# Kernel optimization log

Measured on AMD Instinct MI355X. Metric: run time of the kernel, lower is better.

## Reference

```python
import jax, jax.numpy as jnp
import numpy as np

N, B, E = 2048, 2, 1024      # seq_len, batch, embedding_dims
H = 1024                      # hidden_dims
NH, D = 16, 64                # num_heads, head_dim (NH*D == H)
SCALE = 1.0 / float(np.sqrt(H))  # NOTE: module divides by sqrt(hidden_dims), not sqrt(head_dim)


def setup_inputs() -> dict:
    key = jax.random.key(0)
    k0, k1, k2 = jax.random.split(key, 3)
    x = jax.random.normal(k0, (N, B, E), dtype=jnp.float32)
    W_proj = jax.random.normal(k1, (E, 3 * H), dtype=jnp.float32) * 0.02
    b_proj = jnp.zeros((3 * H,), dtype=jnp.float32)
    W_out = jax.random.normal(k2, (H, E), dtype=jnp.float32) * 0.02
    b_out = jnp.zeros((E,), dtype=jnp.float32)
    return {"x": x, "W_proj": W_proj, "b_proj": b_proj, "W_out": W_out, "b_out": b_out}


def reference(x, W_proj, b_proj, W_out, b_out):
    n, b, _ = x.shape
    # QKV projection: [n, b, 3H] -> 'n b (k h d) -> k b h n d'
    proj = x @ W_proj + b_proj
    qkv = proj.reshape(n, b, 3, NH, D).transpose(2, 1, 3, 0, 4)  # [3, b, h, n, d]
    q, k, v = qkv[0], qkv[1], qkv[2]
    # scaled dot-product scores [b, h, n, n]
    scores = jnp.einsum('bhid,bhjd->bhij', q, k) * SCALE
    # causal mask: -inf above the diagonal (generate_square_subsequent_mask)
    i = jnp.arange(n)
    mask = jnp.where(i[None, :] > i[:, None], -jnp.inf, 0.0).astype(scores.dtype)
    att = jax.nn.softmax(scores + mask, axis=-1)  # dropout = identity (eval)
    out = jnp.einsum('bhij,bhjd->bhid', att, v)   # [b, h, n, d]
    out = out.transpose(2, 0, 1, 3).reshape(n, b, H)  # 'b h n d -> n b (h d)'
    return out @ W_out + b_out
```

## Files before the change

kernel.cpp:

```cpp
#include <hip/hip_runtime.h>
#include <cstdint>
#include <cstddef>

typedef __bf16 bf16_t;
typedef __bf16 bf16x8 __attribute__((ext_vector_type(8)));
typedef __bf16 bf16x4 __attribute__((ext_vector_type(4)));
typedef float f32x4 __attribute__((ext_vector_type(4)));

#define N_SEQ 2048
#define BATCH 2
#define EMB   1024
#define HID   1024
#define NHEAD 16
#define HDIM  64
#define NBROW (N_SEQ * BATCH)
#define ATT_SCALE2 (0.03125f * 1.44269504f)

#define EXP2F(x) __builtin_amdgcn_exp2f(x)

static __device__ __forceinline__ void async_copy16(const bf16_t* g, bf16_t* l) {
  __builtin_amdgcn_global_load_lds((const __attribute__((address_space(1))) void*)g,
                                   (__attribute__((address_space(3))) void*)l,
                                   16, 0, 0);
}

__global__ __launch_bounds__(256) void prep_kernel(
    const float* __restrict__ x, const float* __restrict__ Wp,
    const float* __restrict__ Wo, bf16_t* __restrict__ Xb,
    bf16_t* __restrict__ Wpt, bf16_t* __restrict__ Wot) {
  int bid = blockIdx.x;
  if (bid < 4096) {
    int i = (bid * 256 + threadIdx.x) * 4;
    float4 v = *(const float4*)(x + i);
    bf16x4 o;
    o[0] = (bf16_t)v.x; o[1] = (bf16_t)v.y; o[2] = (bf16_t)v.z; o[3] = (bf16_t)v.w;
    *(bf16x4*)(Xb + i) = o;
    return;
  }
  __shared__ float tile[32][33];
  const float* in; bf16_t* out; int R, C, bx;
  if (bid < 4096 + 3072) { bx = bid - 4096; in = Wp; out = Wpt; R = 1024; C = 3072; }
  else                   { bx = bid - 7168; in = Wo; out = Wot; R = 1024; C = 1024; }
  int gx = C / 32;
  int bc = (bx % gx) * 32, br = (bx / gx) * 32;
  int tx = threadIdx.x & 31, ty = threadIdx.x >> 5;
  #pragma unroll
  for (int i = 0; i < 32; i += 8)
    tile[ty + i][tx] = in[(size_t)(br + ty + i) * C + bc + tx];
  __syncthreads();
  #pragma unroll
  for (int i = 0; i < 32; i += 8)
    out[(size_t)(bc + ty + i) * R + br + tx] = (bf16_t)tile[tx][ty + i];
}

template <int BM, int BN, bool OUT_BF16, bool SCALEQ, bool WRITE_VT>
__global__ __launch_bounds__(256) void gemm_bt_kernel(
    const bf16_t* __restrict__ A, const bf16_t* __restrict__ Bt,
    const float* __restrict__ bias, void* __restrict__ Cout,
    bf16_t* __restrict__ Vt, int M, int Nn, int K) {
  constexpr int BK = 64;
  constexpr int MT = BM / 32;
  constexpr int NT = BN / 32;
  constexpr int CA = BM / 32;
  constexpr int CB = BN / 32;
  constexpr int ASZ = BM * BK;
  constexpr int BSZ = BN * BK;
  __shared__ __align__(16) bf16_t smem[2 * ASZ + 2 * BSZ];
  bf16_t* const Asb = smem;
  bf16_t* const Bsb = smem + 2 * ASZ;
  int tid = threadIdx.x;
  int wave = tid >> 6, lane = tid & 63;
  int c = lane & 15, quad = lane >> 4;
  int bm = blockIdx.x * BM;
  int bn = blockIdx.y * BN;
  int wm = (wave & 1) * (BM / 2), wn = (wave >> 1) * (BN / 2);
  f32x4 acc[MT][NT] = {};

  const bf16_t* agp[CA]; int alo[CA];
  const bf16_t* bgp[CB]; int blo[CB];
  #pragma unroll
  for (int i = 0; i < CA; ++i) {
    int p = i * 256 + tid;
    int row = p >> 3, ko = (p & 7) ^ (row & 7);
    agp[i] = A + (size_t)(bm + row) * K + ko * 8;
    alo[i] = (i * 256 + wave * 64) * 8;
  }
  #pragma unroll
  for (int i = 0; i < CB; ++i) {
    int p = i * 256 + tid;
    int row = p >> 3, ko = (p & 7) ^ (row & 7);
    bgp[i] = Bt + (size_t)(bn + row) * K + ko * 8;
    blo[i] = (i * 256 + wave * 64) * 8;
  }

  #pragma unroll
  for (int i = 0; i < CA; ++i) async_copy16(agp[i], Asb + alo[i]);
  #pragma unroll
  for (int i = 0; i < CB; ++i) async_copy16(bgp[i], Bsb + blo[i]);

  int nkb = K / BK;
  for (int ki = 0; ki < nkb; ++ki) {
    __syncthreads();
    if (ki + 1 < nkb) {
      int kb = (ki + 1) * BK;
      bf16_t* an = Asb + ((ki + 1) & 1) * ASZ;
      bf16_t* bnx = Bsb + ((ki + 1) & 1) * BSZ;
      #pragma unroll
      for (int i = 0; i < CA; ++i) async_copy16(agp[i] + kb, an + alo[i]);
      #pragma unroll
      for (int i = 0; i < CB; ++i) async_copy16(bgp[i] + kb, bnx + blo[i]);
    }
    const bf16_t* as = Asb + (ki & 1) * ASZ;
    const bf16_t* bs = Bsb + (ki & 1) * BSZ;
    #pragma unroll
    for (int kk = 0; kk < 2; ++kk) {
      bf16x8 af[MT], bf[NT];
      #pragma unroll
      for (int mt = 0; mt < MT; ++mt) {
        int row = wm + mt * 16 + c;
        int slot = (kk * 4 + quad) ^ (row & 7);
        af[mt] = *(const bf16x8*)(as + (size_t)(row * 8 + slot) * 8);
      }
      #pragma unroll
      for (int nt = 0; nt < NT; ++nt) {
        int row = wn + nt * 16 + c;
        int slot = (kk * 4 + quad) ^ (row & 7);
        bf[nt] = *(const bf16x8*)(bs + (size_t)(row * 8 + slot) * 8);
      }
      #pragma unroll
      for (int mt = 0; mt < MT; ++mt)
        #pragma unroll
        for (int nt = 0; nt < NT; ++nt)
          acc[mt][nt] = __builtin_amdgcn_mfma_f32_16x16x32_bf16(
              af[mt], bf[nt], acc[mt][nt], 0, 0, 0);
    }
  }

  bool do_vt = WRITE_VT && (bn >= 2 * HID);
  bf16_t* tb = smem;
  if (do_vt) __syncthreads();

  #pragma unroll
  for (int nt = 0; nt < NT; ++nt) {
    int col = bn + wn + nt * 16 + c;
    float bv = bias[col];
    float sc = (SCALEQ && col < HID) ? ATT_SCALE2 : 1.0f;
    #pragma unroll
    for (int mt = 0; mt < MT; ++mt) {
      #pragma unroll
      for (int r = 0; r < 4; ++r) {
        int loc = wm + mt * 16 + quad * 4 + r;
        int row = bm + loc;
        float v = (acc[mt][nt][r] + bv) * sc;
        if (OUT_BF16)
          ((bf16_t*)Cout)[(size_t)row * Nn + col] = (bf16_t)v;
        else
          ((float*)Cout)[(size_t)row * Nn + col] = v;
        if (do_vt) {
          int dg = wn + nt * 16 + c;
          int hh = dg >> 6, dl = dg & 63;
          tb[((loc & 1) * 2 + hh) * 4608 + dl * 72 + (loc >> 1)] = (bf16_t)v;
        }
      }
    }
  }

  if (do_vt) {
    __syncthreads();
    int h0 = (bn - 2 * HID) >> 6;
    int n2 = (tid & 7) * 8;
    #pragma unroll
    for (int i = 0; i < 2; ++i) {
      #pragma unroll
      for (int hh = 0; hh < 2; ++hh) {
        #pragma unroll
        for (int k = 0; k < 2; ++k) {
          int d = (tid >> 3) + k * 32;
          bf16x8 vv = *(const bf16x8*)(tb + ((i * 2 + hh) * 4608) + d * 72 + n2);
          *(bf16x8*)(Vt + (size_t)((i * 16 + h0 + hh) * HDIM + d) * N_SEQ + bm / 2 + n2) = vv;
        }
      }
    }
  }
}

__global__ __launch_bounds__(512, 4) void flash_attn_kernel(
    const bf16_t* __restrict__ Pj, const bf16_t* __restrict__ Vt,
    bf16_t* __restrict__ AO) {
  __shared__ __align__(16) bf16_t Ks[2][64 * 64];
  __shared__ __align__(16) bf16_t Vs[2][64 * 64];
  __shared__ __align__(16) bf16_t Ps[8][16 * 64];
  const int PJP = 3 * HID;
  int tid = threadIdx.x, wave = tid >> 6, lane = tid & 63;
  int c = lane & 15, quad = lane >> 4;
  int c7 = c & 7;
  int bid = blockIdx.x;
  int qb = (bid < 256) ? (15 - (bid >> 5)) : ((bid - 256) >> 5);
  int bh = bid & 31;
  int h = bh & 15, b = bh >> 4;
  int i0 = qb * 128;

  int i_row = i0 + wave * 16 + c;
  const bf16_t* qg = Pj + (size_t)(i_row * BATCH + b) * PJP + h * HDIM + quad * 8;
  bf16x8 qf0 = *(const bf16x8*)(qg);
  bf16x8 qf1 = *(const bf16x8*)(qg + 32);

  f32x4 o[4] = {};
  float lrow = 0.f;

  int jr = tid >> 3, oc = tid & 7;
  int lds_off = jr * 64 + (oc ^ (jr & 7)) * 8;
  const bf16_t* kg0 = Pj + (size_t)b * PJP + HID + h * HDIM + oc * 8;
  const bf16_t* vg0 = Vt + (size_t)(bh * HDIM + jr) * N_SEQ + oc * 8;

  int njt = 2 * qb + 2;
  bf16x8 kreg = *(const bf16x8*)(kg0 + (size_t)jr * BATCH * PJP);
  bf16x8 vreg = *(const bf16x8*)(vg0);

  for (int jt = 0; jt < njt; ++jt) {
    bf16_t* ks = Ks[jt & 1];
    bf16_t* vs = Vs[jt & 1];
    *(bf16x8*)(ks + lds_off) = kreg;
    *(bf16x8*)(vs + lds_off) = vreg;
    __syncthreads();
    if (jt + 1 < njt) {
      int j0n = (jt + 1) * 64;
      kreg = *(const bf16x8*)(kg0 + (size_t)(j0n + jr) * BATCH * PJP);
      vreg = *(const bf16x8*)(vg0 + j0n);
    }

    f32x4 st[4];
    #pragma unroll
    for (int mt = 0; mt < 4; ++mt) {
      const bf16_t* kr = ks + (mt * 16 + c) * 64;
      bf16x8 ka0 = *(const bf16x8*)(kr + ((quad) ^ c7) * 8);
      bf16x8 ka1 = *(const bf16x8*)(kr + ((quad + 4) ^ c7) * 8);
      f32x4 s = {};
      s = __builtin_amdgcn_mfma_f32_16x16x32_bf16(ka0, qf0, s, 0, 0, 0);
      st[mt] = __builtin_amdgcn_mfma_f32_16x16x32_bf16(ka1, qf1, s, 0, 0, 0);
    }
    if (jt >= 2 * qb) {
      int j0 = jt * 64;
      int ig = i0 + wave * 16 + c;
      #pragma unroll
      for (int mt = 0; mt < 4; ++mt)
        #pragma unroll
        for (int r = 0; r < 4; ++r)
          if (j0 + mt * 16 + quad * 4 + r > ig) st[mt][r] = -1e30f;
    }

    #pragma unroll
    for (int mt = 0; mt < 4; ++mt)
      #pragma unroll
      for (int r = 0; r < 4; ++r) {
        st[mt][r] = EXP2F(st[mt][r]);
        lrow += st[mt][r];
      }

    bf16_t* pw = Ps[wave];
    #pragma unroll
    for (int mt = 0; mt < 4; ++mt) {
      bf16x4 pv;
      #pragma unroll
      for (int r = 0; r < 4; ++r) pv[r] = (bf16_t)st[mt][r];
      int joct = mt * 2 + (quad >> 1);
      *(bf16x4*)(pw + c * 64 + (joct ^ c7) * 8 + (quad & 1) * 4) = pv;
    }
    const bf16_t* pr = pw + c * 64;
    bf16x8 pa0 = *(const bf16x8*)(pr + ((quad) ^ c7) * 8);
    bf16x8 pa1 = *(const bf16x8*)(pr + ((quad + 4) ^ c7) * 8);

    #pragma unroll
    for (int nt = 0; nt < 4; ++nt) {
      const bf16_t* vr = vs + (nt * 16 + c) * 64;
      bf16x8 vb0 = *(const bf16x8*)(vr + ((quad) ^ c7) * 8);
      bf16x8 vb1 = *(const bf16x8*)(vr + ((quad + 4) ^ c7) * 8);
      o[nt] = __builtin_amdgcn_mfma_f32_16x16x32_bf16(vb0, pa0, o[nt], 0, 0, 0);
      o[nt] = __builtin_amdgcn_mfma_f32_16x16x32_bf16(vb1, pa1, o[nt], 0, 0, 0);
    }
  }

  float lfull = lrow;
  lfull += __shfl_xor(lfull, 16);
  lfull += __shfl_xor(lfull, 32);
  float linv = 1.0f / lfull;
  int orow = (i0 + wave * 16 + c) * BATCH + b;
  #pragma unroll
  for (int nt = 0; nt < 4; ++nt) {
    bf16x4 pv;
    #pragma unroll
    for (int r = 0; r < 4; ++r) pv[r] = (bf16_t)(o[nt][r] * linv);
    *(bf16x4*)(AO + (size_t)orow * HID + h * HDIM + nt * 16 + quad * 4) = pv;
  }
}

extern "C" void kernel_launch(void* const* d_in, const int* in_sizes, int n_in,
                              void* d_out, int out_size, void* d_ws, size_t ws_size,
                              hipStream_t stream) {
  const float* x      = (const float*)d_in[0];
  const float* W_proj = (const float*)d_in[1];
  const float* b_proj = (const float*)d_in[2];
  const float* W_out  = (const float*)d_in[3];
  const float* b_out  = (const float*)d_in[4];

  bf16_t* Xb  = (bf16_t*)d_ws;
  bf16_t* Wpt = Xb  + (size_t)NBROW * EMB;
  bf16_t* Wot = Wpt + (size_t)3 * HID * EMB;
  bf16_t* Pj  = Wot + (size_t)HID * EMB;
  bf16_t* AO  = Pj  + (size_t)NBROW * 3 * HID;
  bf16_t* Vt  = AO  + (size_t)NBROW * HID;

  prep_kernel<<<8192, 256, 0, stream>>>(x, W_proj, W_out, Xb, Wpt, Wot);
  gemm_bt_kernel<128, 128, true, true, true>
      <<<dim3(NBROW / 128, 3 * HID / 128), 256, 0, stream>>>(
      Xb, Wpt, b_proj, (void*)Pj, Vt, NBROW, 3 * HID, EMB);
  flash_attn_kernel<<<512, 512, 0, stream>>>(Pj, Vt, AO);
  gemm_bt_kernel<128, 128, false, false, false>
      <<<dim3(NBROW / 128, EMB / 128), 256, 0, stream>>>(
      AO, Wot, b_out, d_out, nullptr, NBROW, EMB, HID);
}
```

Before: 160.8 us.

## Rewrite flash attention with 32x32 MFMA, register-resident P and causal tile skip

The attention kernel moves from 16x16x32 to 32x32x16 bf16 MFMA, with each of 4 waves owning 32 query rows instead of 8 waves with 16 rows each, so blocks use 256 threads. The probability tile is repacked into B-operand layout in registers with cross-half lane shuffles, which drops the per-wave LDS round trip for P. Waves skip key tiles that lie entirely above their causal diagonal, and s_setprio is raised around the MFMA bursts. The trade-off is more registers per wave and fewer waves per block, which may lower occupancy and latency hiding.

After: 171.5 us. 6.7% more time.

```diff
diff --git a/kernel.cpp b/kernel.cpp
--- a/kernel.cpp
+++ b/kernel.cpp
@@ -6,6 +6,8 @@
 typedef __bf16 bf16x8 __attribute__((ext_vector_type(8)));
 typedef __bf16 bf16x4 __attribute__((ext_vector_type(4)));
 typedef float f32x4 __attribute__((ext_vector_type(4)));
+typedef float f32x16 __attribute__((ext_vector_type(16)));
+typedef unsigned int u32x4 __attribute__((ext_vector_type(4)));
 
 #define N_SEQ 2048
 #define BATCH 2
@@ -184,113 +186,180 @@
   }
 }
 
-__global__ __launch_bounds__(512, 4) void flash_attn_kernel(
+__global__ __launch_bounds__(256, 3) void flash_attn_kernel(
     const bf16_t* __restrict__ Pj, const bf16_t* __restrict__ Vt,
     bf16_t* __restrict__ AO) {
   __shared__ __align__(16) bf16_t Ks[2][64 * 64];
   __shared__ __align__(16) bf16_t Vs[2][64 * 64];
-  __shared__ __align__(16) bf16_t Ps[8][16 * 64];
   const int PJP = 3 * HID;
   int tid = threadIdx.x, wave = tid >> 6, lane = tid & 63;
-  int c = lane & 15, quad = lane >> 4;
-  int c7 = c & 7;
+  int il = lane & 31, half = lane >> 5;
   int bid = blockIdx.x;
   int qb = (bid < 256) ? (15 - (bid >> 5)) : ((bid - 256) >> 5);
   int bh = bid & 31;
   int h = bh & 15, b = bh >> 4;
   int i0 = qb * 128;
-
-  int i_row = i0 + wave * 16 + c;
-  const bf16_t* qg = Pj + (size_t)(i_row * BATCH + b) * PJP + h * HDIM + quad * 8;
-  bf16x8 qf0 = *(const bf16x8*)(qg);
-  bf16x8 qf1 = *(const bf16x8*)(qg + 32);
-
-  f32x4 o[4] = {};
+  int irow = i0 + wave * 32 + il;
+  int imax = i0 + wave * 32 + 31;
+
+  bf16x8 qf[4];
+  {
+    const bf16_t* qg = Pj + (size_t)(irow * BATCH + b) * PJP + h * HDIM + half * 8;
+    #pragma unroll
+    for (int s = 0; s < 4; ++s) qf[s] = *(const bf16x8*)(qg + s * 16);
+  }
+
+  f32x16 o0 = {}, o1 = {};
   float lrow = 0.f;
 
   int jr = tid >> 3, oc = tid & 7;
-  int lds_off = jr * 64 + (oc ^ (jr & 7)) * 8;
-  const bf16_t* kg0 = Pj + (size_t)b * PJP + HID + h * HDIM + oc * 8;
-  const bf16_t* vg0 = Vt + (size_t)(bh * HDIM + jr) * N_SEQ + oc * 8;
+  int sl = (oc ^ (jr & 7)) * 8;
+  int lo0 = jr * 64 + sl;
+  int lo1 = (jr + 32) * 64 + sl;
+  const bf16_t* kg = Pj + (size_t)b * PJP + HID + h * HDIM + oc * 8;
+  const bf16_t* vg  = Vt + (size_t)(bh * HDIM + jr) * N_SEQ + oc * 8;
+  const bf16_t* vg2 = Vt + (size_t)(bh * HDIM + jr + 32) * N_SEQ + oc * 8;
 
   int njt = 2 * qb + 2;
-  bf16x8 kreg = *(const bf16x8*)(kg0 + (size_t)jr * BATCH * PJP);
-  bf16x8 vreg = *(const bf16x8*)(vg0);
+  bf16x8 k0 = *(const bf16x8*)(kg + (size_t)jr * BATCH * PJP);
+  bf16x8 k1 = *(const bf16x8*)(kg + (size_t)(jr + 32) * BATCH * PJP);
+  bf16x8 v0 = *(const bf16x8*)(vg);
+  bf16x8 v1 = *(const bf16x8*)(vg2);
+
+  int rx = il & 7;
+  bool hb = (half != 0);
 
   for (int jt = 0; jt < njt; ++jt) {
     bf16_t* ks = Ks[jt & 1];
     bf16_t* vs = Vs[jt & 1];
-    *(bf16x8*)(ks + lds_off) = kreg;
-    *(bf16x8*)(vs + lds_off) = vreg;
+    *(bf16x8*)(ks + lo0) = k0;
+    *(bf16x8*)(ks + lo1) = k1;
+    *(bf16x8*)(vs + lo0) = v0;
+    *(bf16x8*)(vs + lo1) = v1;
     __syncthreads();
     if (jt + 1 < njt) {
       int j0n = (jt + 1) * 64;
-      kreg = *(const bf16x8*)(kg0 + (size_t)(j0n + jr) * BATCH * PJP);
-      vreg = *(const bf16x8*)(vg0 + j0n);
-    }
-
-    f32x4 st[4];
-    #pragma unroll
-    for (int mt = 0; mt < 4; ++mt) {
-      const bf16_t* kr = ks + (mt * 16 + c) * 64;
-      bf16x8 ka0 = *(const bf16x8*)(kr + ((quad) ^ c7) * 8);
-      bf16x8 ka1 = *(const bf16x8*)(kr + ((quad + 4) ^ c7) * 8);
-      f32x4 s = {};
-      s = __builtin_amdgcn_mfma_f32_16x16x32_bf16(ka0, qf0, s, 0, 0, 0);
-      st[mt] = __builtin_amdgcn_mfma_f32_16x16x32_bf16(ka1, qf1, s, 0, 0, 0);
-    }
-    if (jt >= 2 * qb) {
-      int j0 = jt * 64;
-      int ig = i0 + wave * 16 + c;
-      #pragma unroll
-      for (int mt = 0; mt < 4; ++mt)
+      k0 = *(const bf16x8*)(kg + (size_t)(j0n + jr) * BATCH * PJP);
+      k1 = *(const bf16x8*)(kg + (size_t)(j0n + jr + 32) * BATCH * PJP);
+      v0 = *(const bf16x8*)(vg + j0n);
+      v1 = *(const bf16x8*)(vg2 + j0n);
+    }
+
+    if (jt * 64 <= imax) {
+      f32x16 st0 = {}, st1 = {};
+      __builtin_amdgcn_s_setprio(1);
+      #pragma unroll
+      for (int s = 0; s < 4; ++s) {
+        bf16x8 ka = *(const bf16x8*)(ks + il * 64 + (((half + 2 * s) & 7) ^ rx) * 8);
+        st0 = __builtin_amdgcn_mfma_f32_32x32x16_bf16(ka, qf[s], st0, 0, 0, 0);
+      }
+      #pragma unroll
+      for (int s = 0; s < 4; ++s) {
+        bf16x8 ka = *(const bf16x8*)(ks + (32 + il) * 64 + (((half + 2 * s) & 7) ^ rx) * 8);
+        st1 = __builtin_amdgcn_mfma_f32_32x32x16_bf16(ka, qf[s], st1, 0, 0, 0);
+      }
+      __builtin_amdgcn_s_setprio(0);
+
+      if (jt >= 2 * qb) {
+        int j0 = jt * 64;
         #pragma unroll
-        for (int r = 0; r < 4; ++r)
-          if (j0 + mt * 16 + quad * 4 + r > ig) st[mt][r] = -1e30f;
-    }
-
-    #pragma unroll
-    for (int mt = 0; mt < 4; ++mt)
-      #pragma unroll
-      for (int r = 0; r < 4; ++r) {
-        st[mt][r] = EXP2F(st[mt][r]);
-        lrow += st[mt][r];
-      }
-
-    bf16_t* pw = Ps[wave];
-    #pragma unroll
-    for (int mt = 0; mt < 4; ++mt) {
-      bf16x4 pv;
-      #pragma unroll
-      for (int r = 0; r < 4; ++r) pv[r] = (bf16_t)st[mt][r];
-      int joct = mt * 2 + (quad >> 1);
-      *(bf16x4*)(pw + c * 64 + (joct ^ c7) * 8 + (quad & 1) * 4) = pv;
-    }
-    const bf16_t* pr = pw + c * 64;
-    bf16x8 pa0 = *(const bf16x8*)(pr + ((quad) ^ c7) * 8);
-    bf16x8 pa1 = *(const bf16x8*)(pr + ((quad + 4) ^ c7) * 8);
-
-    #pragma unroll
-    for (int nt = 0; nt < 4; ++nt) {
-      const bf16_t* vr = vs + (nt * 16 + c) * 64;
-      bf16x8 vb0 = *(const bf16x8*)(vr + ((quad) ^ c7) * 8);
-      bf16x8 vb1 = *(const bf16x8*)(vr + ((quad + 4) ^ c7) * 8);
-      o[nt] = __builtin_amdgcn_mfma_f32_16x16x32_bf16(vb0, pa0, o[nt], 0, 0, 0);
-      o[nt] = __builtin_amdgcn_mfma_f32_16x16x32_bf16(vb1, pa1, o[nt], 0, 0, 0);
-    }
-  }
-
-  float lfull = lrow;
-  lfull += __shfl_xor(lfull, 16);
-  lfull += __shfl_xor(lfull, 32);
-  float linv = 1.0f / lfull;
-  int orow = (i0 + wave * 16 + c) * BATCH + b;
-  #pragma unroll
-  for (int nt = 0; nt < 4; ++nt) {
-    bf16x4 pv;
-    #pragma unroll
-    for (int r = 0; r < 4; ++r) pv[r] = (bf16_t)(o[nt][r] * linv);
-    *(bf16x4*)(AO + (size_t)orow * HID + h * HDIM + nt * 16 + quad * 4) = pv;
+        for (int r = 0; r < 16; ++r) {
+          int jrow = (r & 3) + 8 * (r >> 2) + 4 * half;
+          if (j0 + jrow > irow)      st0[r] = -1e30f;
+          if (j0 + 32 + jrow > irow) st1[r] = -1e30f;
+        }
+      }
+
+      #pragma unroll
+      for (int r = 0; r < 16; ++r) {
+        st0[r] = EXP2F(st0[r]); lrow += st0[r];
+        st1[r] = EXP2F(st1[r]); lrow += st1[r];
+      }
+
+      unsigned int fr[4][4];
+      #pragma unroll
+      for (int t = 0; t < 2; ++t) {
+        {
+          unsigned int lw0, lw1, hw0, hw1;
+          {
+            unsigned short a0 = __builtin_bit_cast(unsigned short, (bf16_t)st0[8*t+0]);
+            unsigned short a1 = __builtin_bit_cast(unsigned short, (bf16_t)st0[8*t+1]);
+            unsigned short a2 = __builtin_bit_cast(unsigned short, (bf16_t)st0[8*t+2]);
+            unsigned short a3 = __builtin_bit_cast(unsigned short, (bf16_t)st0[8*t+3]);
+            unsigned short a4 = __builtin_bit_cast(unsigned short, (bf16_t)st0[8*t+4]);
+            unsigned short a5 = __builtin_bit_cast(unsigned short, (bf16_t)st0[8*t+5]);
+            unsigned short a6 = __builtin_bit_cast(unsigned short, (bf16_t)st0[8*t+6]);
+            unsigned short a7 = __builtin_bit_cast(unsigned short, (bf16_t)st0[8*t+7]);
+            lw0 = (unsigned int)a0 | ((unsigned int)a1 << 16);
+            lw1 = (unsigned int)a2 | ((unsigned int)a3 << 16);
+            hw0 = (unsigned int)a4 | ((unsigned int)a5 << 16);
+            hw1 = (unsigned int)a6 | ((unsigned int)a7 << 16);
+          }
+          unsigned int pl0 = (unsigned int)__shfl_xor((int)lw0, 32);
+          unsigned int pl1 = (unsigned int)__shfl_xor((int)lw1, 32);
+          unsigned int ph0 = (unsigned int)__shfl_xor((int)hw0, 32);
+          unsigned int ph1 = (unsigned int)__shfl_xor((int)hw1, 32);
+          fr[t][0] = hb ? ph0 : lw0;
+          fr[t][1] = hb ? ph1 : lw1;
+          fr[t][2] = hb ? hw0 : pl0;
+          fr[t][3] = hb ? hw1 : pl1;
+        }
+        {
+          unsigned int lw0, lw1, hw0, hw1;
+          {
+            unsigned short a0 = __builtin_bit_cast(unsigned short, (bf16_t)st1[8*t+0]);
+            unsigned short a1 = __builtin_bit_cast(unsigned short, (bf16_t)st1[8*t+1]);
+            unsigned short a2 = __builtin_bit_cast(unsigned short, (bf16_t)st1[8*t+2]);
+            unsigned short a3 = __builtin_bit_cast(unsigned short, (bf16_t)st1[8*t+3]);
+            unsigned short a4 = __builtin_bit_cast(unsigned short, (bf16_t)st1[8*t+4]);
+            unsigned short a5 = __builtin_bit_cast(unsigned short, (bf16_t)st1[8*t+5]);
+            unsigned short a6 = __builtin_bit_cast(unsigned short, (bf16_t)st1[8*t+6]);
+            unsigned short a7 = __builtin_bit_cast(unsigned short, (bf16_t)st1[8*t+7]);
+            lw0 = (unsigned int)a0 | ((unsigned int)a1 << 16);
+            lw1 = (unsigned int)a2 | ((unsigned int)a3 << 16);
+            hw0 = (unsigned int)a4 | ((unsigned int)a5 << 16);
+            hw1 = (unsigned int)a6 | ((unsigned int)a7 << 16);
+          }
+          unsigned int pl0 = (unsigned int)__shfl_xor((int)lw0, 32);
+          unsigned int pl1 = (unsigned int)__shfl_xor((int)lw1, 32);
+          unsigned int ph0 = (unsigned int)__shfl_xor((int)hw0, 32);
+          unsigned int ph1 = (unsigned int)__shfl_xor((int)hw1, 32);
+          fr[2 + t][0] = hb ? ph0 : lw0;
+          fr[2 + t][1] = hb ? ph1 : lw1;
+          fr[2 + t][2] = hb ? hw0 : pl0;
+          fr[2 + t][3] = hb ? hw1 : pl1;
+        }
+      }
+
+      __builtin_amdgcn_s_setprio(1);
+      #pragma unroll
+      for (int s = 0; s < 4; ++s) {
+        u32x4 w = {fr[s][0], fr[s][1], fr[s][2], fr[s][3]};
+        bf16x8 pb = __builtin_bit_cast(bf16x8, w);
+        bf16x8 va0 = *(const bf16x8*)(vs + il * 64 + (((half + 2 * s) & 7) ^ rx) * 8);
+        bf16x8 va1 = *(const bf16x8*)(vs + (32 + il) * 64 + (((half + 2 * s) & 7) ^ rx) * 8);
+        o0 = __builtin_amdgcn_mfma_f32_32x32x16_bf16(va0, pb, o0, 0, 0, 0);
+        o1 = __builtin_amdgcn_mfma_f32_32x32x16_bf16(va1, pb, o1, 0, 0, 0);
+      }
+      __builtin_amdgcn_s_setprio(0);
+    }
+  }
+
+  lrow += __shfl_xor(lrow, 32);
+  float linv = 1.0f / lrow;
+  int orow = irow * BATCH + b;
+  bf16_t* ao = AO + (size_t)orow * HID + h * HDIM;
+  #pragma unroll
+  for (int t = 0; t < 4; ++t) {
+    bf16x4 pv0, pv1;
+    #pragma unroll
+    for (int r2 = 0; r2 < 4; ++r2) {
+      pv0[r2] = (bf16_t)(o0[t * 4 + r2] * linv);
+      pv1[r2] = (bf16_t)(o1[t * 4 + r2] * linv);
+    }
+    int d0 = t * 8 + 4 * half;
+    *(bf16x4*)(ao + d0) = pv0;
+    *(bf16x4*)(ao + 32 + d0) = pv1;
   }
 }
 
@@ -314,7 +383,7 @@
   gemm_bt_kernel<128, 128, true, true, true>
       <<<dim3(NBROW / 128, 3 * HID / 128), 256, 0, stream>>>(
       Xb, Wpt, b_proj, (void*)Pj, Vt, NBROW, 3 * HID, EMB);
-  flash_attn_kernel<<<512, 512, 0, stream>>>(Pj, Vt, AO);
+  flash_attn_kernel<<<512, 256, 0, stream>>>(Pj, Vt, AO);
   gemm_bt_kernel<128, 128, false, false, false>
       <<<dim3(NBROW / 128, EMB / 128), 256, 0, stream>>>(
       AO, Wot, b_out, d_out, nullptr, NBROW, EMB, HID);
```

## Double KV tile to 128 keys per iteration and skip masked diagonal sub-tiles

Applied to the files above, without the earlier changes.

The flash attention loop now processes 128 keys per iteration instead of 64, which halves the number of barriers and loop iterations. The V tile layout is widened to 128 columns with an XOR swizzle. On the diagonal tile, each wave skips the QK MFMAs and the second PV half for key sub-tiles that are fully masked. The larger LDS buffers and the extra registers for st[8] lower the occupancy hint from 4 to 2 blocks per CU, so less latency can be hidden by other blocks.

Result: slower. 172.1 us (+7.0%).

```diff
diff --git a/kernel.cpp b/kernel.cpp
--- a/kernel.cpp
+++ b/kernel.cpp
@@ -184,11 +184,11 @@
   }
 }
 
-__global__ __launch_bounds__(512, 4) void flash_attn_kernel(
+__global__ __launch_bounds__(512, 2) void flash_attn_kernel(
     const bf16_t* __restrict__ Pj, const bf16_t* __restrict__ Vt,
     bf16_t* __restrict__ AO) {
-  __shared__ __align__(16) bf16_t Ks[2][64 * 64];
-  __shared__ __align__(16) bf16_t Vs[2][64 * 64];
+  __shared__ __align__(16) bf16_t Ks[2][128 * 64];
+  __shared__ __align__(16) bf16_t Vs[2][64 * 128];
   __shared__ __align__(16) bf16_t Ps[8][16 * 64];
   const int PJP = 3 * HID;
   int tid = threadIdx.x, wave = tid >> 6, lane = tid & 63;
@@ -209,48 +209,64 @@
   float lrow = 0.f;
 
   int jr = tid >> 3, oc = tid & 7;
-  int lds_off = jr * 64 + (oc ^ (jr & 7)) * 8;
-  const bf16_t* kg0 = Pj + (size_t)b * PJP + HID + h * HDIM + oc * 8;
-  const bf16_t* vg0 = Vt + (size_t)(bh * HDIM + jr) * N_SEQ + oc * 8;
-
-  int njt = 2 * qb + 2;
-  bf16x8 kreg = *(const bf16x8*)(kg0 + (size_t)jr * BATCH * PJP);
-  bf16x8 vreg = *(const bf16x8*)(vg0);
+  int ko0 = jr * 64 + (oc ^ (jr & 7)) * 8;
+  int ko1 = (jr + 64) * 64 + (oc ^ (jr & 7)) * 8;
+  const bf16_t* kg = Pj + (size_t)b * PJP + HID + h * HDIM + oc * 8;
+  int d0 = tid >> 4, joct = tid & 15;
+  int vo0 = d0 * 128 + (joct ^ (d0 & 7)) * 8;
+  int vo1 = (d0 + 32) * 128 + (joct ^ (d0 & 7)) * 8;
+  const bf16_t* vg0 = Vt + (size_t)(bh * HDIM + d0) * N_SEQ + joct * 8;
+  const bf16_t* vg1 = Vt + (size_t)(bh * HDIM + d0 + 32) * N_SEQ + joct * 8;
+
+  int njt = qb + 1;
+  bf16x8 kr0 = *(const bf16x8*)(kg + (size_t)jr * BATCH * PJP);
+  bf16x8 kr1 = *(const bf16x8*)(kg + (size_t)(jr + 64) * BATCH * PJP);
+  bf16x8 vr0 = *(const bf16x8*)(vg0);
+  bf16x8 vr1 = *(const bf16x8*)(vg1);
 
   for (int jt = 0; jt < njt; ++jt) {
     bf16_t* ks = Ks[jt & 1];
     bf16_t* vs = Vs[jt & 1];
-    *(bf16x8*)(ks + lds_off) = kreg;
-    *(bf16x8*)(vs + lds_off) = vreg;
+    *(bf16x8*)(ks + ko0) = kr0;
+    *(bf16x8*)(ks + ko1) = kr1;
+    *(bf16x8*)(vs + vo0) = vr0;
+    *(bf16x8*)(vs + vo1) = vr1;
     __syncthreads();
     if (jt + 1 < njt) {
-      int j0n = (jt + 1) * 64;
-      kreg = *(const bf16x8*)(kg0 + (size_t)(j0n + jr) * BATCH * PJP);
-      vreg = *(const bf16x8*)(vg0 + j0n);
-    }
-
-    f32x4 st[4];
-    #pragma unroll
-    for (int mt = 0; mt < 4; ++mt) {
-      const bf16_t* kr = ks + (mt * 16 + c) * 64;
-      bf16x8 ka0 = *(const bf16x8*)(kr + ((quad) ^ c7) * 8);
-      bf16x8 ka1 = *(const bf16x8*)(kr + ((quad + 4) ^ c7) * 8);
-      f32x4 s = {};
-      s = __builtin_amdgcn_mfma_f32_16x16x32_bf16(ka0, qf0, s, 0, 0, 0);
-      st[mt] = __builtin_amdgcn_mfma_f32_16x16x32_bf16(ka1, qf1, s, 0, 0, 0);
-    }
-    if (jt >= 2 * qb) {
-      int j0 = jt * 64;
-      int ig = i0 + wave * 16 + c;
-      #pragma unroll
-      for (int mt = 0; mt < 4; ++mt)
+      int j0n = (jt + 1) * 128;
+      kr0 = *(const bf16x8*)(kg + (size_t)(j0n + jr) * BATCH * PJP);
+      kr1 = *(const bf16x8*)(kg + (size_t)(j0n + jr + 64) * BATCH * PJP);
+      vr0 = *(const bf16x8*)(vg0 + j0n);
+      vr1 = *(const bf16x8*)(vg1 + j0n);
+    }
+
+    bool diag = (jt == qb);
+    f32x4 st[8];
+    #pragma unroll
+    for (int mt = 0; mt < 8; ++mt) {
+      if (!diag || mt <= wave) {
+        const bf16_t* kr = ks + (mt * 16 + c) * 64;
+        bf16x8 ka0 = *(const bf16x8*)(kr + ((quad) ^ c7) * 8);
+        bf16x8 ka1 = *(const bf16x8*)(kr + ((quad + 4) ^ c7) * 8);
+        f32x4 s = {};
+        s = __builtin_amdgcn_mfma_f32_16x16x32_bf16(ka0, qf0, s, 0, 0, 0);
+        st[mt] = __builtin_amdgcn_mfma_f32_16x16x32_bf16(ka1, qf1, s, 0, 0, 0);
+      } else {
+        st[mt][0] = -1e30f; st[mt][1] = -1e30f;
+        st[mt][2] = -1e30f; st[mt][3] = -1e30f;
+      }
+    }
+    if (diag) {
+      int il = wave * 16 + c;
+      #pragma unroll
+      for (int mt = 0; mt < 8; ++mt)
         #pragma unroll
         for (int r = 0; r < 4; ++r)
-          if (j0 + mt * 16 + quad * 4 + r > ig) st[mt][r] = -1e30f;
-    }
-
-    #pragma unroll
-    for (int mt = 0; mt < 4; ++mt)
+          if (mt * 16 + quad * 4 + r > il) st[mt][r] = -1e30f;
+    }
+
+    #pragma unroll
+    for (int mt = 0; mt < 8; ++mt)
       #pragma unroll
       for (int r = 0; r < 4; ++r) {
         st[mt][r] = EXP2F(st[mt][r]);
@@ -259,24 +275,30 @@
 
     bf16_t* pw = Ps[wave];
     #pragma unroll
-    for (int mt = 0; mt < 4; ++mt) {
-      bf16x4 pv;
-      #pragma unroll
-      for (int r = 0; r < 4; ++r) pv[r] = (bf16_t)st[mt][r];
-      int joct = mt * 2 + (quad >> 1);
-      *(bf16x4*)(pw + c * 64 + (joct ^ c7) * 8 + (quad & 1) * 4) = pv;
-    }
-    const bf16_t* pr = pw + c * 64;
-    bf16x8 pa0 = *(const bf16x8*)(pr + ((quad) ^ c7) * 8);
-    bf16x8 pa1 = *(const bf16x8*)(pr + ((quad + 4) ^ c7) * 8);
-
-    #pragma unroll
-    for (int nt = 0; nt < 4; ++nt) {
-      const bf16_t* vr = vs + (nt * 16 + c) * 64;
-      bf16x8 vb0 = *(const bf16x8*)(vr + ((quad) ^ c7) * 8);
-      bf16x8 vb1 = *(const bf16x8*)(vr + ((quad + 4) ^ c7) * 8);
-      o[nt] = __builtin_amdgcn_mfma_f32_16x16x32_bf16(vb0, pa0, o[nt], 0, 0, 0);
-      o[nt] = __builtin_amdgcn_mfma_f32_16x16x32_bf16(vb1, pa1, o[nt], 0, 0, 0);
+    for (int hf = 0; hf < 2; ++hf) {
+      if (hf == 0 || !diag || wave >= 4) {
+        #pragma unroll
+        for (int mtl = 0; mtl < 4; ++mtl) {
+          f32x4 sv = st[hf * 4 + mtl];
+          bf16x4 pv;
+          #pragma unroll
+          for (int r = 0; r < 4; ++r) pv[r] = (bf16_t)sv[r];
+          int jo = mtl * 2 + (quad >> 1);
+          *(bf16x4*)(pw + c * 64 + (jo ^ c7) * 8 + (quad & 1) * 4) = pv;
+        }
+        const bf16_t* pr = pw + c * 64;
+        bf16x8 pa0 = *(const bf16x8*)(pr + ((quad) ^ c7) * 8);
+        bf16x8 pa1 = *(const bf16x8*)(pr + ((quad + 4) ^ c7) * 8);
+        #pragma unroll
+        for (int nt = 0; nt < 4; ++nt) {
+          const bf16_t* vrp = vs + (nt * 16 + c) * 128;
+          bf16x8 va0 = *(const bf16x8*)(vrp + ((hf * 8 + quad) ^ c7) * 8);
+          bf16x8 va1 = *(const bf16x8*)(vrp + ((hf * 8 + 4 + quad) ^ c7) * 8);
+          o[nt] = __builtin_amdgcn_mfma_f32_16x16x32_bf16(va0, pa0, o[nt], 0, 0, 0);
+          o[nt] = __builtin_amdgcn_mfma_f32_16x16x32_bf16(va1, pa1, o[nt], 0, 0, 0);
+        }
+        asm volatile("" ::: "memory");
+      }
     }
   }
 
```

## Add dedicated QKV GEMM with triple-buffered async LDS pipeline and BK=32

Applied to the files above, without the earlier changes.

Replaces the templated QKV projection GEMM with a specialized kernel that uses BK=32 tiles, a 3-stage ring of LDS buffers filled by async global-to-LDS copies, and a swizzled layout. Only one barrier per k-step is needed, with explicit vmcnt waits keeping two stages in flight. The Q scaling and V-transpose epilogue are kept, and the generic GEMM drops its template flags. The deeper prefetch aims to hide global load latency, at the cost of more barriers per K and a larger LDS footprint per stage count.

After: 161.9 us. About the same (+0.7%).

```diff
diff --git a/kernel.cpp b/kernel.cpp
--- a/kernel.cpp
+++ b/kernel.cpp
@@ -53,11 +53,130 @@
     out[(size_t)(bc + ty + i) * R + br + tx] = (bf16_t)tile[tx][ty + i];
 }
 
-template <int BM, int BN, bool OUT_BF16, bool SCALEQ, bool WRITE_VT>
+__global__ __launch_bounds__(256) void gemm_qkv_kernel(
+    const bf16_t* __restrict__ A, const bf16_t* __restrict__ Bt,
+    const float* __restrict__ bias, bf16_t* __restrict__ Cout,
+    bf16_t* __restrict__ Vt, int Nn, int K) {
+  constexpr int BM = 128, BN = 128, BK = 32;
+  constexpr int TSZ = BM * BK;
+  __shared__ __align__(16) bf16_t smem[3 * 2 * TSZ];
+  int tid = threadIdx.x;
+  int wave = tid >> 6, lane = tid & 63;
+  int c = lane & 15, quad = lane >> 4;
+  int bm = blockIdx.x * BM;
+  int bn = blockIdx.y * BN;
+  int wm = (wave & 1) * 64, wn = (wave >> 1) * 64;
+  f32x4 acc[4][4] = {};
+
+  const bf16_t* agp[2]; const bf16_t* bgp[2]; int ldo[2];
+  #pragma unroll
+  for (int i = 0; i < 2; ++i) {
+    int p = i * 256 + tid;
+    int row = p >> 2;
+    int ko = (p & 3) ^ ((row >> 1) & 3);
+    agp[i] = A + (size_t)(bm + row) * K + ko * 8;
+    bgp[i] = Bt + (size_t)(bn + row) * K + ko * 8;
+    ldo[i] = (i * 256 + wave * 64) * 8;
+  }
+
+  auto stage = [&](int s) {
+    bf16_t* ab = smem + (s % 3) * 2 * TSZ;
+    bf16_t* bb = ab + TSZ;
+    int ks = s * BK;
+    #pragma unroll
+    for (int i = 0; i < 2; ++i) {
+      async_copy16(agp[i] + ks, ab + ldo[i]);
+      async_copy16(bgp[i] + ks, bb + ldo[i]);
+    }
+  };
+
+  auto compute = [&](int s) {
+    const bf16_t* ab = smem + (s % 3) * 2 * TSZ;
+    const bf16_t* bb = ab + TSZ;
+    bf16x8 af[4], bf[4];
+    #pragma unroll
+    for (int mt = 0; mt < 4; ++mt) {
+      int row = wm + mt * 16 + c;
+      int slot = (quad ^ (row >> 1)) & 3;
+      af[mt] = *(const bf16x8*)(ab + row * 32 + slot * 8);
+    }
+    #pragma unroll
+    for (int nt = 0; nt < 4; ++nt) {
+      int row = wn + nt * 16 + c;
+      int slot = (quad ^ (row >> 1)) & 3;
+      bf[nt] = *(const bf16x8*)(bb + row * 32 + slot * 8);
+    }
+    #pragma unroll
+    for (int mt = 0; mt < 4; ++mt)
+      #pragma unroll
+      for (int nt = 0; nt < 4; ++nt)
+        acc[mt][nt] = __builtin_amdgcn_mfma_f32_16x16x32_bf16(
+            af[mt], bf[nt], acc[mt][nt], 0, 0, 0);
+  };
+
+  int nkb = K / BK;
+  stage(0); stage(1);
+  for (int s = 0; s < nkb - 1; ++s) {
+    asm volatile("s_waitcnt vmcnt(4)" ::: "memory");
+    __builtin_amdgcn_s_barrier();
+    asm volatile("" ::: "memory");
+    if (s + 2 < nkb) stage(s + 2);
+    compute(s);
+  }
+  asm volatile("s_waitcnt vmcnt(0)" ::: "memory");
+  __builtin_amdgcn_s_barrier();
+  asm volatile("" ::: "memory");
+  compute(nkb - 1);
+
+  bool do_vt = (bn >= 2 * HID);
+  bf16_t* tb = smem;
+  __syncthreads();
+
+  #pragma unroll
+  for (int nt = 0; nt < 4; ++nt) {
+    int col = bn + wn + nt * 16 + c;
+    float bv = bias[col];
+    float sc = (col < HID) ? ATT_SCALE2 : 1.0f;
+    #pragma unroll
+    for (int mt = 0; mt < 4; ++mt) {
+      #pragma unroll
+      for (int r = 0; r < 4; ++r) {
+        int loc = wm + mt * 16 + quad * 4 + r;
+        float v = (acc[mt][nt][r] + bv) * sc;
+        Cout[(size_t)(bm + loc) * Nn + col] = (bf16_t)v;
+        if (do_vt) {
+          int dg = wn + nt * 16 + c;
+          int hh = dg >> 6, dl = dg & 63;
+          tb[((loc & 1) * 2 + hh) * 4608 + dl * 72 + (loc >> 1)] = (bf16_t)v;
+        }
+      }
+    }
+  }
+
+  if (do_vt) {
+    __syncthreads();
+    int h0 = (bn - 2 * HID) >> 6;
+    int n2 = (tid & 7) * 8;
+    #pragma unroll
+    for (int i = 0; i < 2; ++i) {
+      #pragma unroll
+      for (int hh = 0; hh < 2; ++hh) {
+        #pragma unroll
+        for (int k = 0; k < 2; ++k) {
+          int d = (tid >> 3) + k * 32;
+          bf16x8 vv = *(const bf16x8*)(tb + ((i * 2 + hh) * 4608) + d * 72 + n2);
+          *(bf16x8*)(Vt + (size_t)((i * 16 + h0 + hh) * HDIM + d) * N_SEQ + bm / 2 + n2) = vv;
+        }
+      }
+    }
+  }
+}
+
+template <int BM, int BN, bool OUT_BF16>
 __global__ __launch_bounds__(256) void gemm_bt_kernel(
     const bf16_t* __restrict__ A, const bf16_t* __restrict__ Bt,
     const float* __restrict__ bias, void* __restrict__ Cout,
-    bf16_t* __restrict__ Vt, int M, int Nn, int K) {
+    int M, int Nn, int K) {
   constexpr int BK = 64;
   constexpr int MT = BM / 32;
   constexpr int NT = BN / 32;
@@ -136,49 +255,21 @@
     }
   }
 
-  bool do_vt = WRITE_VT && (bn >= 2 * HID);
-  bf16_t* tb = smem;
-  if (do_vt) __syncthreads();
-
   #pragma unroll
   for (int nt = 0; nt < NT; ++nt) {
     int col = bn + wn + nt * 16 + c;
     float bv = bias[col];
-    float sc = (SCALEQ && col < HID) ? ATT_SCALE2 : 1.0f;
     #pragma unroll
     for (int mt = 0; mt < MT; ++mt) {
       #pragma unroll
       for (int r = 0; r < 4; ++r) {
         int loc = wm + mt * 16 + quad * 4 + r;
         int row = bm + loc;
-        float v = (acc[mt][nt][r] + bv) * sc;
+        float v = acc[mt][nt][r] + bv;
         if (OUT_BF16)
           ((bf16_t*)Cout)[(size_t)row * Nn + col] = (bf16_t)v;
         else
           ((float*)Cout)[(size_t)row * Nn + col] = v;
-        if (do_vt) {
-          int dg = wn + nt * 16 + c;
-          int hh = dg >> 6, dl = dg & 63;
-          tb[((loc & 1) * 2 + hh) * 4608 + dl * 72 + (loc >> 1)] = (bf16_t)v;
-        }
-      }
-    }
-  }
-
-  if (do_vt) {
-    __syncthreads();
-    int h0 = (bn - 2 * HID) >> 6;
-    int n2 = (tid & 7) * 8;
-    #pragma unroll
-    for (int i = 0; i < 2; ++i) {
-      #pragma unroll
-      for (int hh = 0; hh < 2; ++hh) {
-        #pragma unroll
-        for (int k = 0; k < 2; ++k) {
-          int d = (tid >> 3) + k * 32;
-          bf16x8 vv = *(const bf16x8*)(tb + ((i * 2 + hh) * 4608) + d * 72 + n2);
-          *(bf16x8*)(Vt + (size_t)((i * 16 + h0 + hh) * HDIM + d) * N_SEQ + bm / 2 + n2) = vv;
-        }
       }
     }
   }
@@ -311,11 +402,10 @@
   bf16_t* Vt  = AO  + (size_t)NBROW * HID;
 
   prep_kernel<<<8192, 256, 0, stream>>>(x, W_proj, W_out, Xb, Wpt, Wot);
-  gemm_bt_kernel<128, 128, true, true, true>
-      <<<dim3(NBROW / 128, 3 * HID / 128), 256, 0, stream>>>(
-      Xb, Wpt, b_proj, (void*)Pj, Vt, NBROW, 3 * HID, EMB);
+  gemm_qkv_kernel<<<dim3(NBROW / 128, 3 * HID / 128), 256, 0, stream>>>(
+      Xb, Wpt, b_proj, Pj, Vt, 3 * HID, EMB);
   flash_attn_kernel<<<512, 512, 0, stream>>>(Pj, Vt, AO);
-  gemm_bt_kernel<128, 128, false, false, false>
+  gemm_bt_kernel<128, 128, false>
       <<<dim3(NBROW / 128, EMB / 128), 256, 0, stream>>>(
-      AO, Wot, b_out, d_out, nullptr, NBROW, EMB, HID);
-}
+      AO, Wot, b_out, d_out, NBROW, EMB, HID);
+}
```
